# Kernel tuning notes

Hardware: AMD Instinct MI355X
Metric: run time of the kernel (lower is better)

The kernel has to match this reference:

```python
import jax, jax.numpy as jnp
import numpy as np

N = 50000      # nodes
E = 800000     # edges
F_IN = 128     # input node features
HID = 96       # hidden_channels (heads=1 -> in_dim=HID)
L = 4          # num_layers
OUT = 1
EPS_SM = 1e-16 # PyG softmax eps


def layer_norm(x, g, b):
    mu = jnp.mean(x, axis=-1, keepdims=True)
    var = jnp.var(x, axis=-1, keepdims=True)
    return (x - mu) * jax.lax.rsqrt(var + 1e-5) * g + b


def gatv2_layer(h, src, dst, ea, Wl, bl, Wr, br, We, att, bias):
    # GATv2Conv, heads=1, concat=True, add_self_loops=False, edge_dim=1
    xl = h @ Wl + bl                      # [N, C] source transform (x_j)
    xr = h @ Wr + br                      # [N, C] target transform (x_i)
    e = xl[src] + xr[dst] + ea @ We       # [E, C]
    e = jax.nn.leaky_relu(e, 0.2)
    alpha = e @ att                       # [E]
    # softmax over incoming edges of each destination node
    m = jax.ops.segment_max(alpha, dst, num_segments=N)
    a = jnp.exp(alpha - m[dst])
    s = jax.ops.segment_sum(a, dst, num_segments=N)
    a = a / (s[dst] + EPS_SM)
    out = jax.ops.segment_sum(xl[src] * a[:, None], dst, num_segments=N)
    return out + bias


def setup_inputs() -> dict:
    key = jax.random.key(0)
    ks = jax.random.split(key, 24)
    sc_in = 1.0 / np.sqrt(F_IN)
    sc_h = 1.0 / np.sqrt(HID)
    inp = {
        "x": jax.random.normal(ks[0], (N, F_IN), jnp.float32),
        "edge_index": jax.random.randint(ks[1], (2, E), 0, N, jnp.int64),
        "edge_weight": jax.random.uniform(ks[2], (E,), jnp.float32),
        "enc_W": jax.random.normal(ks[3], (F_IN, HID), jnp.float32) * sc_in,
        "enc_b": jnp.zeros((HID,), jnp.float32),
        "Wl": jax.random.normal(ks[4], (L, HID, HID), jnp.float32) * sc_h,
        "bl": jnp.zeros((L, HID), jnp.float32),
        "Wr": jax.random.normal(ks[5], (L, HID, HID), jnp.float32) * sc_h,
        "br": jnp.zeros((L, HID), jnp.float32),
        "We": jax.random.normal(ks[6], (L, 1, HID), jnp.float32),
        "att": jax.random.normal(ks[7], (L, HID), jnp.float32) * sc_h,
        "bias": jnp.zeros((L, HID), jnp.float32),
        "ln_g": jnp.ones((L, HID), jnp.float32),
        "ln_b": jnp.zeros((L, HID), jnp.float32),
        "lnf_g": jnp.ones((HID,), jnp.float32),
        "lnf_b": jnp.zeros((HID,), jnp.float32),
        "fc_W": jax.random.normal(ks[8], (HID, OUT), jnp.float32) * sc_h,
        "fc_b": jnp.zeros((OUT,), jnp.float32),
    }
    return inp


def reference(x, edge_index, edge_weight, enc_W, enc_b, Wl, bl, Wr, br, We, att,
              bias, ln_g, ln_b, lnf_g, lnf_b, fc_W, fc_b):
    src, dst = edge_index[0], edge_index[1]
    ea = edge_weight[:, None]             # [E, 1] edge_attr
    h = x @ enc_W + enc_b                 # node encoder
    for i in range(L):                    # DeepGCNLayer block='res+'
        hn = jax.nn.relu(layer_norm(h, ln_g[i], ln_b[i]))
        h = h + gatv2_layer(hn, src, dst, ea, Wl[i], bl[i], Wr[i], br[i],
                            We[i], att[i], bias[i])
    h = jax.nn.relu(layer_norm(h, lnf_g, lnf_b))
    return h @ fc_W + fc_b
```

## Files before the change

### kernel.cpp

```cpp
#include <hip/hip_runtime.h>
#include <math.h>

#define NN 50000
#define EE 800000
#define FIN 128
#define HID 96
#define NL 4
#define CHUNK 1024

typedef __attribute__((ext_vector_type(8))) short short8;
typedef __attribute__((ext_vector_type(4))) float floatx4;
typedef __attribute__((ext_vector_type(2))) _Float16 half2v;

#define WPREP_L (NL * 2 * 9216)
#define WPREP_TOT (WPREP_L + 12288)

#define PH1E 4096
#define NBUCK 98
#define BCAP 9216

struct u96 { unsigned x, y, z; };

__device__ __forceinline__ unsigned short f32_to_bf16_rne(float x) {
    unsigned u = __float_as_uint(x);
    unsigned r = (u + 0x7FFFu + ((u >> 16) & 1u)) >> 16;
    return (unsigned short)r;
}
__device__ __forceinline__ float bf16_to_f32(unsigned short h) {
    return __uint_as_float(((unsigned)h) << 16);
}

__global__ void k_hist(const int* __restrict__ dst, int* __restrict__ deg, int E) {
    int e = blockIdx.x * blockDim.x + threadIdx.x;
    if (e < E) atomicAdd(&deg[dst[e]], 1);
}

__global__ void k_scan1(const int* __restrict__ deg, int* __restrict__ partials, int n) {
    __shared__ int lds[256];
    int t = threadIdx.x;
    int base = blockIdx.x * CHUNK + t * 4;
    int s = 0;
    #pragma unroll
    for (int q = 0; q < 4; q++) { int idx = base + q; if (idx < n) s += deg[idx]; }
    lds[t] = s; __syncthreads();
    for (int o = 128; o > 0; o >>= 1) { if (t < o) lds[t] += lds[t + o]; __syncthreads(); }
    if (t == 0) partials[blockIdx.x] = lds[0];
}

__global__ void k_scan_mid(int* partials, int nb, int* rowptr, int n) {
    int lane = threadIdx.x;
    int orig = (lane < nb) ? partials[lane] : 0;
    int v = orig;
    #pragma unroll
    for (int off = 1; off < 64; off <<= 1) {
        int u = __shfl_up(v, off);
        if (lane >= off) v += u;
    }
    if (lane < nb) partials[lane] = v - orig;
    if (lane == 63) rowptr[n] = v;
}

__global__ void k_scan3(const int* __restrict__ deg, const int* __restrict__ partials,
                        int* __restrict__ rowptr, int* __restrict__ cursor, int n) {
    __shared__ int lds[256];
    int t = threadIdx.x;
    int base = blockIdx.x * CHUNK + t * 4;
    int v[4];
    #pragma unroll
    for (int q = 0; q < 4; q++) { int idx = base + q; v[q] = (idx < n) ? deg[idx] : 0; }
    int tsum = v[0] + v[1] + v[2] + v[3];
    lds[t] = tsum; __syncthreads();
    for (int o = 1; o < 256; o <<= 1) {
        int add = (t >= o) ? lds[t - o] : 0;
        __syncthreads();
        lds[t] += add;
        __syncthreads();
    }
    int excl = lds[t] - tsum;
    int run = partials[blockIdx.x] + excl;
    #pragma unroll
    for (int q = 0; q < 4; q++) {
        int idx = base + q;
        if (idx < n) { rowptr[idx] = run; cursor[idx] = run; run += v[q]; }
    }
}

__global__ __launch_bounds__(256) void k_binscatter(const int* __restrict__ src,
        const int* __restrict__ dst, const float* __restrict__ ew,
        int* __restrict__ gcur, uint2* __restrict__ ibuf, int E) {
    __shared__ uint2 st[PH1E];
    __shared__ int cnt[NBUCK], off[NBUCK], cur[NBUCK], gbase[NBUCK];
    int t = threadIdx.x;
    int e0 = blockIdx.x * PH1E;
    for (int i = t; i < NBUCK; i += 256) { cnt[i] = 0; cur[i] = 0; }
    __syncthreads();
    #pragma unroll
    for (int k = 0; k < PH1E / 256; k++) {
        int e = e0 + k * 256 + t;
        if (e < E) atomicAdd(&cnt[dst[e] >> 9], 1);
    }
    __syncthreads();
    if (t == 0) {
        int run = 0;
        for (int b = 0; b < NBUCK; b++) { off[b] = run; run += cnt[b]; }
    }
    __syncthreads();
    #pragma unroll
    for (int k = 0; k < PH1E / 256; k++) {
        int e = e0 + k * 256 + t;
        if (e < E) {
            int d = dst[e];
            int b = d >> 9;
            int p = off[b] + atomicAdd(&cur[b], 1);
            _Float16 hw = (_Float16)ew[e];
            unsigned short wb = *(unsigned short*)&hw;
            st[p] = make_uint2((unsigned)d, (unsigned)src[e] | ((unsigned)wb << 16));
        }
    }
    __syncthreads();
    if (t < NBUCK) gbase[t] = atomicAdd(&gcur[t], cur[t]);
    __syncthreads();
    int total = min(PH1E, E - e0);
    for (int i = t; i < total; i += 256) {
        uint2 v = st[i];
        int b = v.x >> 9;
        ibuf[(size_t)b * BCAP + gbase[b] + (i - off[b])] = v;
    }
}

__global__ __launch_bounds__(256) void k_binplace(const uint2* __restrict__ ibuf,
        const int* __restrict__ gcur, const int* __restrict__ rowptr,
        unsigned* __restrict__ epack, int n) {
    __shared__ int cur[512];
    int t = threadIdx.x;
    int b = blockIdx.x;
    int n0 = b << 9;
    for (int i = t; i < 512; i += 256) {
        int node = n0 + i;
        cur[i] = (node < n) ? rowptr[node] : 0;
    }
    __syncthreads();
    int nb = gcur[b];
    for (int i = t; i < nb; i += 256) {
        uint2 v = ibuf[(size_t)b * BCAP + i];
        int p = atomicAdd(&cur[(int)v.x - n0], 1);
        epack[p] = v.y;
    }
}

__global__ void k_wprep_all(const float* __restrict__ Wl, const float* __restrict__ Wr,
                            const float* __restrict__ encW,
                            unsigned short* __restrict__ wf_hi, unsigned short* __restrict__ wf_lo,
                            unsigned short* __restrict__ we_hi, unsigned short* __restrict__ we_lo) {
    int t = blockIdx.x * blockDim.x + threadIdx.x;
    if (t < WPREP_L) {
        int within = t % 9216, pair = t / 9216;
        int lr = pair & 1, layer = pair >> 1;
        int j = within & 7;
        int lane = (within >> 3) & 63;
        int cs = within >> 9;
        int s = cs % 3, ct = cs / 3;
        int col = ct * 16 + (lane & 15);
        int k = s * 32 + (lane >> 4) * 8 + j;
        const float* W = (lr ? Wr : Wl) + (size_t)layer * HID * HID;
        float v = W[k * HID + col];
        unsigned short hi = f32_to_bf16_rne(v);
        wf_hi[t] = hi;
        wf_lo[t] = f32_to_bf16_rne(v - bf16_to_f32(hi));
    } else if (t < WPREP_TOT) {
        int u = t - WPREP_L;
        int j = u & 7;
        int lane = (u >> 3) & 63;
        int cs = u >> 9;
        int s = cs & 3, ct = cs >> 2;
        int col = ct * 16 + (lane & 15);
        int k = s * 32 + (lane >> 4) * 8 + j;
        float v = encW[k * HID + col];
        unsigned short hi = f32_to_bf16_rne(v);
        we_hi[u] = hi;
        we_lo[u] = f32_to_bf16_rne(v - bf16_to_f32(hi));
    }
}

__global__ __launch_bounds__(256) void k_enc_mfma(const float* __restrict__ x,
        const unsigned short* __restrict__ we_hi, const unsigned short* __restrict__ we_lo,
        const float* __restrict__ b,
        const float* __restrict__ lng, const float* __restrict__ lnb,
        float* __restrict__ h,
        unsigned short* __restrict__ hn_hi, unsigned short* __restrict__ hn_lo, int n) {
    int t = threadIdx.x;
    int wave = t >> 6, lane = t & 63;
    int quad = lane >> 4, lid = lane & 15;
    int r0 = blockIdx.x * 64 + wave * 16;
    int arow = r0 + lid; if (arow >= n) arow = n - 1;
    short8 aH[4], aL[4];
    #pragma unroll
    for (int s = 0; s < 4; s++) {
        float4 p0 = *(const float4*)(x + (size_t)arow * FIN + s * 32 + quad * 8);
        float4 p1 = *(const float4*)(x + (size_t)arow * FIN + s * 32 + quad * 8 + 4);
        float f[8] = {p0.x, p0.y, p0.z, p0.w, p1.x, p1.y, p1.z, p1.w};
        #pragma unroll
        for (int j = 0; j < 8; j++) {
            unsigned short hi = f32_to_bf16_rne(f[j]);
            aH[s][j] = (short)hi;
            aL[s][j] = (short)f32_to_bf16_rne(f[j] - bf16_to_f32(hi));
        }
    }
    floatx4 o[6];
    #pragma unroll
    for (int ct = 0; ct < 6; ct++) {
        floatx4 acc = {0.f, 0.f, 0.f, 0.f};
        #pragma unroll
        for (int s = 0; s < 4; s++) {
            short8 bH = *(const short8*)(we_hi + ((ct * 4 + s) * 64 + lane) * 8);
            short8 bL = *(const short8*)(we_lo + ((ct * 4 + s) * 64 + lane) * 8);
            acc = __builtin_amdgcn_mfma_f32_16x16x32_bf16(aH[s], bH, acc, 0, 0, 0);
            acc = __builtin_amdgcn_mfma_f32_16x16x32_bf16(aH[s], bL, acc, 0, 0, 0);
            acc = __builtin_amdgcn_mfma_f32_16x16x32_bf16(aL[s], bH, acc, 0, 0, 0);
        }
        float bv = b[ct * 16 + lid];
        #pragma unroll
        for (int rg = 0; rg < 4; rg++) o[ct][rg] = acc[rg] + bv;
    }
    #pragma unroll
    for (int rg = 0; rg < 4; rg++) {
        float s1 = 0.f, s2 = 0.f;
        #pragma unroll
        for (int ct = 0; ct < 6; ct++) { s1 += o[ct][rg]; s2 += o[ct][rg] * o[ct][rg]; }
        #pragma unroll
        for (int off = 1; off < 16; off <<= 1) {
            s1 += __shfl_xor(s1, off);
            s2 += __shfl_xor(s2, off);
        }
        float mu = s1 * (1.f / 96.f);
        float var = s2 * (1.f / 96.f) - mu * mu;
        float rs = rsqrtf(var + 1e-5f);
        int orow = r0 + quad * 4 + rg;
        if (orow < n) {
            #pragma unroll
            for (int ct = 0; ct < 6; ct++) {
                int col = ct * 16 + lid;
                float v = o[ct][rg];
                h[(size_t)orow * HID + col] = v;
                float y = fmaxf((v - mu) * rs * lng[col] + lnb[col], 0.f);
                unsigned short hi = f32_to_bf16_rne(y);
                hn_hi[(size_t)orow * HID + col] = hi;
                hn_lo[(size_t)orow * HID + col] = f32_to_bf16_rne(y - bf16_to_f32(hi));
            }
        }
    }
}

__global__ __launch_bounds__(256) void k_gemm2_mfma(
        const unsigned short* __restrict__ hn_hi, const unsigned short* __restrict__ hn_lo,
        const unsigned short* __restrict__ wf_hi, const unsigned short* __restrict__ wf_lo,
        const float* __restrict__ bl, const float* __restrict__ br,
        unsigned short* __restrict__ xl_h, unsigned short* __restrict__ xr_h, int n) {
    __shared__ unsigned short lh[9216];
    __shared__ unsigned short ll[9216];
    int t = threadIdx.x;
    int wave = t >> 6, lane = t & 63;
    int quad = lane >> 4, lid = lane & 15;
    int r0 = blockIdx.x * 64 + wave * 16;
    int arow = r0 + lid; if (arow >= n) arow = n - 1;
    short8 aH[3], aL[3];
    #pragma unroll
    for (int s = 0; s < 3; s++) {
        aH[s] = *(const short8*)(hn_hi + (size_t)arow * HID + s * 32 + quad * 8);
        aL[s] = *(const short8*)(hn_lo + (size_t)arow * HID + s * 32 + quad * 8);
    }
    for (int lr = 0; lr < 2; lr++) {
        const unsigned short* sh = wf_hi + lr * 9216;
        const unsigned short* sl = wf_lo + lr * 9216;
        __syncthreads();
        for (int u = t; u < 1152; u += 256) {
            *(short8*)(lh + u * 8) = *(const short8*)(sh + u * 8);
            *(short8*)(ll + u * 8) = *(const short8*)(sl + u * 8);
        }
        __syncthreads();
        const float* bias = lr ? br : bl;
        unsigned short* out = lr ? xr_h : xl_h;
        #pragma unroll
        for (int ct = 0; ct < 6; ct++) {
            floatx4 acc = {0.f, 0.f, 0.f, 0.f};
            #pragma unroll
            for (int s = 0; s < 3; s++) {
                short8 bH = *(const short8*)(lh + ((ct * 3 + s) * 64 + lane) * 8);
                short8 bL = *(const short8*)(ll + ((ct * 3 + s) * 64 + lane) * 8);
                acc = __builtin_amdgcn_mfma_f32_16x16x32_bf16(aH[s], bH, acc, 0, 0, 0);
                acc = __builtin_amdgcn_mfma_f32_16x16x32_bf16(aH[s], bL, acc, 0, 0, 0);
                acc = __builtin_amdgcn_mfma_f32_16x16x32_bf16(aL[s], bH, acc, 0, 0, 0);
            }
            int col = ct * 16 + lid;
            float bv = bias[col];
            #pragma unroll
            for (int rg = 0; rg < 4; rg++) {
                int orow = r0 + quad * 4 + rg;
                if (orow < n) {
                    _Float16 hv = (_Float16)(acc[rg] + bv);
                    out[(size_t)orow * HID + col] = *(unsigned short*)&hv;
                }
            }
        }
    }
}

__global__ __launch_bounds__(256) void k_gat_fused(
        const unsigned short* __restrict__ xl_h, const unsigned short* __restrict__ xr_h,
        const unsigned* __restrict__ ep, const int* __restrict__ rowptr,
        const float* __restrict__ We, const float* __restrict__ att, const float* __restrict__ bias,
        float* __restrict__ h,
        unsigned short* __restrict__ hn_hi, unsigned short* __restrict__ hn_lo,
        float* __restrict__ out_final,
        const float* __restrict__ g, const float* __restrict__ bt,
        const float* __restrict__ fcW, const float* __restrict__ fcb,
        int mode, int n) {
    int lane = threadIdx.x & 63;
    int node = blockIdx.x * 4 + (threadIdx.x >> 6);
    if (node >= n) return;
    int grp = lane >> 4, sub = lane & 15;
    int d0 = sub * 6;
    unsigned gOffB = (unsigned)(sub * 12);

    const float LOG2E = 1.4426950408889634f;
    union U6 { u96 u; half2v h2[3]; _Float16 hf[6]; };
    half2v we_h[3], at_h[3], xr_hv[3];
    {
        U6 xrw;
        xrw.u = *(const u96*)((const char*)xr_h + ((unsigned)node * 192u + gOffB));
        float2 a0 = *(const float2*)(We + d0);
        float2 a1 = *(const float2*)(We + d0 + 2);
        float2 a2 = *(const float2*)(We + d0 + 4);
        float2 c0 = *(const float2*)(att + d0);
        float2 c1 = *(const float2*)(att + d0 + 2);
        float2 c2 = *(const float2*)(att + d0 + 4);
        we_h[0] = half2v{(_Float16)a0.x, (_Float16)a0.y};
        we_h[1] = half2v{(_Float16)a1.x, (_Float16)a1.y};
        we_h[2] = half2v{(_Float16)a2.x, (_Float16)a2.y};
        at_h[0] = half2v{(_Float16)(c0.x*LOG2E), (_Float16)(c0.y*LOG2E)};
        at_h[1] = half2v{(_Float16)(c1.x*LOG2E), (_Float16)(c1.y*LOG2E)};
        at_h[2] = half2v{(_Float16)(c2.x*LOG2E), (_Float16)(c2.y*LOG2E)};
        #pragma unroll
        for (int j = 0; j < 3; j++) xr_hv[j] = xrw.h2[j];
    }
    const half2v c02 = half2v{(_Float16)0.2f, (_Float16)0.2f};

    int beg = rowptr[node], end = rowptr[node + 1];
    float ssum = 0.f;
    float acc[6];
    #pragma unroll
    for (int j = 0; j < 6; j++) acc[j] = 0.f;

    auto lq = [&](int p, u96& vraw, _Float16& wh, bool& val) {
        int pe = p + grp;
        val = pe < end;
        int pc = val ? pe : end - 1;
        unsigned e = ep[pc];
        unsigned short wb = (unsigned short)(e >> 16);
        wh = *(_Float16*)&wb;
        vraw = *(const u96*)((const char*)xl_h + ((e & 0xFFFFu) * 192u + gOffB));
    };
    auto proc = [&](const u96& vraw, _Float16 wh, bool val) {
        U6 cv; cv.u = vraw;
        half2v w2 = half2v{wh, wh};
        float q = 0.f;
        #pragma unroll
        for (int j = 0; j < 3; j++) {
            half2v t = cv.h2[j] + xr_hv[j];
            t = w2 * we_h[j] + t;
            half2v t2 = t * c02;
            t = __builtin_elementwise_max(t, t2);
#if __has_builtin(__builtin_amdgcn_fdot2)
            q = __builtin_amdgcn_fdot2(t, at_h[j], q, false);
#else
            q = fmaf((float)t[0], (float)at_h[j][0], q);
            q = fmaf((float)t[1], (float)at_h[j][1], q);
#endif
        }
        q += __shfl_xor(q, 1); q += __shfl_xor(q, 2);
        q += __shfl_xor(q, 4); q += __shfl_xor(q, 8);
        float e = val ? exp2f(q) : 0.f;
        ssum += e;
        #pragma unroll
        for (int j = 0; j < 6; j++) acc[j] = fmaf((float)cv.hf[j], e, acc[j]);
    };

    if (beg < end) {
        u96 vA, vB; _Float16 wA, wB; bool okA, okB;
        lq(beg,     vA, wA, okA);
        lq(beg + 4, vB, wB, okB);
        for (int p = beg; p < end; p += 8) {
            proc(vA, wA, okA);
            lq(p + 8, vA, wA, okA);
            proc(vB, wB, okB);
            lq(p + 12, vB, wB, okB);
        }
    }

    ssum += __shfl_xor(ssum, 16); ssum += __shfl_xor(ssum, 32);
    #pragma unroll
    for (int j = 0; j < 6; j++) {
        acc[j] += __shfl_xor(acc[j], 16);
        acc[j] += __shfl_xor(acc[j], 32);
    }
    float inv = 1.f / (ssum + 1e-16f);

    float nh[6];
    float s1 = 0.f, s2 = 0.f;
    {
        float2 h0 = *(const float2*)(h + (size_t)node * HID + d0);
        float2 h1 = *(const float2*)(h + (size_t)node * HID + d0 + 2);
        float2 h2 = *(const float2*)(h + (size_t)node * HID + d0 + 4);
        float2 b0 = *(const float2*)(bias + d0);
        float2 b1 = *(const float2*)(bias + d0 + 2);
        float2 b2 = *(const float2*)(bias + d0 + 4);
        float hv[6] = {h0.x, h0.y, h1.x, h1.y, h2.x, h2.y};
        float bv[6] = {b0.x, b0.y, b1.x, b1.y, b2.x, b2.y};
        #pragma unroll
        for (int j = 0; j < 6; j++) {
            nh[j] = hv[j] + acc[j] * inv + bv[j];
            s1 += nh[j];
            s2 += nh[j] * nh[j];
        }
    }
    #pragma unroll
    for (int off = 1; off < 16; off <<= 1) {
        s1 += __shfl_xor(s1, off);
        s2 += __shfl_xor(s2, off);
    }
    float mu = s1 * (1.f / 96.f);
    float var = s2 * (1.f / 96.f) - mu * mu;
    float rs = rsqrtf(var + 1e-5f);

    if (mode == 0) {
        if (grp == 0) {
            float2 g0 = *(const float2*)(g + d0);
            float2 g1 = *(const float2*)(g + d0 + 2);
            float2 g2 = *(const float2*)(g + d0 + 4);
            float2 t0 = *(const float2*)(bt + d0);
            float2 t1 = *(const float2*)(bt + d0 + 2);
            float2 t2 = *(const float2*)(bt + d0 + 4);
            float gv[6] = {g0.x, g0.y, g1.x, g1.y, g2.x, g2.y};
            float tv[6] = {t0.x, t0.y, t1.x, t1.y, t2.x, t2.y};
            *(float2*)(h + (size_t)node * HID + d0)     = make_float2(nh[0], nh[1]);
            *(float2*)(h + (size_t)node * HID + d0 + 2) = make_float2(nh[2], nh[3]);
            *(float2*)(h + (size_t)node * HID + d0 + 4) = make_float2(nh[4], nh[5]);
            unsigned hi[3], lo[3];
            #pragma unroll
            for (int j = 0; j < 3; j++) {
                float ox = fmaxf((nh[2*j]   - mu) * rs * gv[2*j]   + tv[2*j],   0.f);
                float oy = fmaxf((nh[2*j+1] - mu) * rs * gv[2*j+1] + tv[2*j+1], 0.f);
                unsigned short hx = f32_to_bf16_rne(ox), hy = f32_to_bf16_rne(oy);
                unsigned short lx = f32_to_bf16_rne(ox - bf16_to_f32(hx));
                unsigned short ly = f32_to_bf16_rne(oy - bf16_to_f32(hy));
                hi[j] = (unsigned)hx | ((unsigned)hy << 16);
                lo[j] = (unsigned)lx | ((unsigned)ly << 16);
            }
            u96 wh = {hi[0], hi[1], hi[2]};
            u96 wl = {lo[0], lo[1], lo[2]};
            *(u96*)((char*)hn_hi + 2 * ((size_t)node * HID + d0)) = wh;
            *(u96*)((char*)hn_lo + 2 * ((size_t)node * HID + d0)) = wl;
        }
    } else {
        float pacc = 0.f;
        {
            float2 g0 = *(const float2*)(g + d0);
            float2 g1 = *(const float2*)(g + d0 + 2);
            float2 g2 = *(const float2*)(g + d0 + 4);
            float2 t0 = *(const float2*)(bt + d0);
            float2 t1 = *(const float2*)(bt + d0 + 2);
            float2 t2 = *(const float2*)(bt + d0 + 4);
            float2 w0 = *(const float2*)(fcW + d0);
            float2 w1 = *(const float2*)(fcW + d0 + 2);
            float2 w2 = *(const float2*)(fcW + d0 + 4);
            float gv[6] = {g0.x, g0.y, g1.x, g1.y, g2.x, g2.y};
            float tv[6] = {t0.x, t0.y, t1.x, t1.y, t2.x, t2.y};
            float wv[6] = {w0.x, w0.y, w1.x, w1.y, w2.x, w2.y};
            #pragma unroll
            for (int j = 0; j < 6; j++) {
                float y = fmaxf((nh[j] - mu) * rs * gv[j] + tv[j], 0.f);
                pacc = fmaf(y, wv[j], pacc);
            }
        }
        #pragma unroll
        for (int off = 1; off < 16; off <<= 1) pacc += __shfl_xor(pacc, off);
        if (lane == 0) out_final[node] = pacc + fcb[0];
    }
}

extern "C" void kernel_launch(void* const* d_in, const int* in_sizes, int n_in,
                              void* d_out, int out_size, void* d_ws, size_t ws_size,
                              hipStream_t stream) {
    const float* x    = (const float*)d_in[0];
    const int*   ei   = (const int*)  d_in[1];
    const float* ew   = (const float*)d_in[2];
    const float* encW = (const float*)d_in[3];
    const float* encB = (const float*)d_in[4];
    const float* Wl   = (const float*)d_in[5];
    const float* bl   = (const float*)d_in[6];
    const float* Wr   = (const float*)d_in[7];
    const float* br   = (const float*)d_in[8];
    const float* We   = (const float*)d_in[9];
    const float* att  = (const float*)d_in[10];
    const float* bias = (const float*)d_in[11];
    const float* lng  = (const float*)d_in[12];
    const float* lnb  = (const float*)d_in[13];
    const float* lnfg = (const float*)d_in[14];
    const float* lnfb = (const float*)d_in[15];
    const float* fcW  = (const float*)d_in[16];
    const float* fcb  = (const float*)d_in[17];
    float* out = (float*)d_out;

    const int* src = ei;
    const int* dst = ei + EE;

    char* ws = (char*)d_ws;
    size_t off = 0;
    auto alloc = [&](size_t bytes) -> void* {
        void* p = ws + off;
        off += (bytes + 255) & ~(size_t)255;
        return p;
    };
    float* h      = (float*)alloc((size_t)NN * HID * 4);
    unsigned short* xl_h  = (unsigned short*)alloc((size_t)NN * HID * 2 + 256);
    unsigned short* xr_h  = (unsigned short*)alloc((size_t)NN * HID * 2 + 256);
    unsigned short* hn_hi = (unsigned short*)alloc((size_t)NN * HID * 2);
    unsigned short* hn_lo = (unsigned short*)alloc((size_t)NN * HID * 2);
    unsigned short* wf_hi = (unsigned short*)alloc((size_t)WPREP_L * 2);
    unsigned short* wf_lo = (unsigned short*)alloc((size_t)WPREP_L * 2);
    unsigned short* we_hi = (unsigned short*)alloc(12288 * 2);
    unsigned short* we_lo = (unsigned short*)alloc(12288 * 2);
    int*   deg    = (int*)  alloc((size_t)NN * 4);
    int*   rowptr = (int*)  alloc((size_t)(NN + 1) * 4);
    int*   cursor = (int*)  alloc((size_t)NN * 4);
    unsigned* epack = (unsigned*)alloc((size_t)EE * 4);
    uint2* ibuf   = (uint2*)alloc((size_t)NBUCK * BCAP * 8);
    int*   gcur   = (int*)  alloc(NBUCK * 4);
    int*   parts  = (int*)  alloc(256 * 4);

    const int NB = (NN + CHUNK - 1) / CHUNK;
    const int EB = (EE + 255) / 256;
    const int PB = (EE + PH1E - 1) / PH1E;
    const int MB = (NN + 63) / 64;
    const int WB = (NN + 3) / 4;

    hipMemsetAsync(deg, 0, (size_t)NN * 4, stream);
    hipMemsetAsync(gcur, 0, NBUCK * 4, stream);
    k_hist<<<EB, 256, 0, stream>>>(dst, deg, EE);
    k_binscatter<<<PB, 256, 0, stream>>>(src, dst, ew, gcur, ibuf, EE);
    k_scan1<<<NB, 256, 0, stream>>>(deg, parts, NN);
    k_scan_mid<<<1, 64, 0, stream>>>(parts, NB, rowptr, NN);
    k_scan3<<<NB, 256, 0, stream>>>(deg, parts, rowptr, cursor, NN);
    k_binplace<<<NBUCK, 256, 0, stream>>>(ibuf, gcur, rowptr, epack, NN);

    k_wprep_all<<<(WPREP_TOT + 255) / 256, 256, 0, stream>>>(Wl, Wr, encW, wf_hi, wf_lo, we_hi, we_lo);

    k_enc_mfma<<<MB, 256, 0, stream>>>(x, we_hi, we_lo, encB, lng, lnb, h, hn_hi, hn_lo, NN);

    for (int l = 0; l < NL; l++) {
        k_gemm2_mfma<<<MB, 256, 0, stream>>>(hn_hi, hn_lo,
            wf_hi + (size_t)l * 2 * 9216, wf_lo + (size_t)l * 2 * 9216,
            bl + l * HID, br + l * HID, xl_h, xr_h, NN);
        if (l < NL - 1) {
            k_gat_fused<<<WB, 256, 0, stream>>>(xl_h, xr_h, epack, rowptr,
                We + l * HID, att + l * HID, bias + l * HID,
                h, hn_hi, hn_lo, (float*)nullptr,
                lng + (l + 1) * HID, lnb + (l + 1) * HID,
                (const float*)nullptr, (const float*)nullptr, 0, NN);
        } else {
            k_gat_fused<<<WB, 256, 0, stream>>>(xl_h, xr_h, epack, rowptr,
                We + l * HID, att + l * HID, bias + l * HID,
                h, (unsigned short*)nullptr, (unsigned short*)nullptr, out,
                lnfg, lnfb, fcW, fcb, 1, NN);
        }
    }
}
```

Measured before the change: 451.3 us.

## Replace split-bf16 triple MFMA with single fp16 MFMA and fold degree histogram

Switches the node encoder and per-layer dual GEMMs from a hi/lo bf16 split (three MFMAs per step, two activation buffers, two weight copies) to one fp16 MFMA with a single fp16 activation and weight buffer. This halves hn read/write traffic in the GAT epilogue and GEMM, halves LDS weight staging, and cuts MFMA count by a factor of three. It also moves the in-degree histogram into the bin-scatter kernel, dropping one launch and one extra pass over dst. The cost is lower matmul precision (fp16 with 10-bit mantissa instead of near-fp32 split) and possible fp16 range limits.

```diff
diff --git a/kernel.cpp b/kernel.cpp
--- a/kernel.cpp
+++ b/kernel.cpp
@@ -21,18 +21,9 @@
 
 struct u96 { unsigned x, y, z; };
 
-__device__ __forceinline__ unsigned short f32_to_bf16_rne(float x) {
-    unsigned u = __float_as_uint(x);
-    unsigned r = (u + 0x7FFFu + ((u >> 16) & 1u)) >> 16;
-    return (unsigned short)r;
-}
-__device__ __forceinline__ float bf16_to_f32(unsigned short h) {
-    return __uint_as_float(((unsigned)h) << 16);
-}
-
-__global__ void k_hist(const int* __restrict__ dst, int* __restrict__ deg, int E) {
-    int e = blockIdx.x * blockDim.x + threadIdx.x;
-    if (e < E) atomicAdd(&deg[dst[e]], 1);
+__device__ __forceinline__ unsigned short f16bits(float x) {
+    _Float16 h = (_Float16)x;
+    return *(unsigned short*)&h;
 }
 
 __global__ void k_scan1(const int* __restrict__ deg, int* __restrict__ partials, int n) {
@@ -87,7 +78,7 @@
 
 __global__ __launch_bounds__(256) void k_binscatter(const int* __restrict__ src,
         const int* __restrict__ dst, const float* __restrict__ ew,
-        int* __restrict__ gcur, uint2* __restrict__ ibuf, int E) {
+        int* __restrict__ deg, int* __restrict__ gcur, uint2* __restrict__ ibuf, int E) {
     __shared__ uint2 st[PH1E];
     __shared__ int cnt[NBUCK], off[NBUCK], cur[NBUCK], gbase[NBUCK];
     int t = threadIdx.x;
@@ -97,7 +88,11 @@
     #pragma unroll
     for (int k = 0; k < PH1E / 256; k++) {
         int e = e0 + k * 256 + t;
-        if (e < E) atomicAdd(&cnt[dst[e] >> 9], 1);
+        if (e < E) {
+            int d = dst[e];
+            atomicAdd(&cnt[d >> 9], 1);
+            atomicAdd(&deg[d], 1);
+        }
     }
     __syncthreads();
     if (t == 0) {
@@ -112,8 +107,7 @@
             int d = dst[e];
             int b = d >> 9;
             int p = off[b] + atomicAdd(&cur[b], 1);
-            _Float16 hw = (_Float16)ew[e];
-            unsigned short wb = *(unsigned short*)&hw;
+            unsigned short wb = f16bits(ew[e]);
             st[p] = make_uint2((unsigned)d, (unsigned)src[e] | ((unsigned)wb << 16));
         }
     }
@@ -150,8 +144,7 @@
 
 __global__ void k_wprep_all(const float* __restrict__ Wl, const float* __restrict__ Wr,
                             const float* __restrict__ encW,
-                            unsigned short* __restrict__ wf_hi, unsigned short* __restrict__ wf_lo,
-                            unsigned short* __restrict__ we_hi, unsigned short* __restrict__ we_lo) {
+                            unsigned short* __restrict__ wf, unsigned short* __restrict__ we) {
     int t = blockIdx.x * blockDim.x + threadIdx.x;
     if (t < WPREP_L) {
         int within = t % 9216, pair = t / 9216;
@@ -163,10 +156,7 @@
         int col = ct * 16 + (lane & 15);
         int k = s * 32 + (lane >> 4) * 8 + j;
         const float* W = (lr ? Wr : Wl) + (size_t)layer * HID * HID;
-        float v = W[k * HID + col];
-        unsigned short hi = f32_to_bf16_rne(v);
-        wf_hi[t] = hi;
-        wf_lo[t] = f32_to_bf16_rne(v - bf16_to_f32(hi));
+        wf[t] = f16bits(W[k * HID + col]);
     } else if (t < WPREP_TOT) {
         int u = t - WPREP_L;
         int j = u & 7;
@@ -175,36 +165,29 @@
         int s = cs & 3, ct = cs >> 2;
         int col = ct * 16 + (lane & 15);
         int k = s * 32 + (lane >> 4) * 8 + j;
-        float v = encW[k * HID + col];
-        unsigned short hi = f32_to_bf16_rne(v);
-        we_hi[u] = hi;
-        we_lo[u] = f32_to_bf16_rne(v - bf16_to_f32(hi));
+        we[u] = f16bits(encW[k * HID + col]);
     }
 }
 
 __global__ __launch_bounds__(256) void k_enc_mfma(const float* __restrict__ x,
-        const unsigned short* __restrict__ we_hi, const unsigned short* __restrict__ we_lo,
+        const unsigned short* __restrict__ we,
         const float* __restrict__ b,
         const float* __restrict__ lng, const float* __restrict__ lnb,
         float* __restrict__ h,
-        unsigned short* __restrict__ hn_hi, unsigned short* __restrict__ hn_lo, int n) {
+        unsigned short* __restrict__ hn, int n) {
     int t = threadIdx.x;
     int wave = t >> 6, lane = t & 63;
     int quad = lane >> 4, lid = lane & 15;
     int r0 = blockIdx.x * 64 + wave * 16;
     int arow = r0 + lid; if (arow >= n) arow = n - 1;
-    short8 aH[4], aL[4];
+    short8 aF[4];
     #pragma unroll
     for (int s = 0; s < 4; s++) {
         float4 p0 = *(const float4*)(x + (size_t)arow * FIN + s * 32 + quad * 8);
         float4 p1 = *(const float4*)(x + (size_t)arow * FIN + s * 32 + quad * 8 + 4);
         float f[8] = {p0.x, p0.y, p0.z, p0.w, p1.x, p1.y, p1.z, p1.w};
         #pragma unroll
-        for (int j = 0; j < 8; j++) {
-            unsigned short hi = f32_to_bf16_rne(f[j]);
-            aH[s][j] = (short)hi;
-            aL[s][j] = (short)f32_to_bf16_rne(f[j] - bf16_to_f32(hi));
-        }
+        for (int j = 0; j < 8; j++) aF[s][j] = (short)f16bits(f[j]);
     }
     floatx4 o[6];
     #pragma unroll
@@ -212,11 +195,8 @@
         floatx4 acc = {0.f, 0.f, 0.f, 0.f};
         #pragma unroll
         for (int s = 0; s < 4; s++) {
-            short8 bH = *(const short8*)(we_hi + ((ct * 4 + s) * 64 + lane) * 8);
-            short8 bL = *(const short8*)(we_lo + ((ct * 4 + s) * 64 + lane) * 8);
-            acc = __builtin_amdgcn_mfma_f32_16x16x32_bf16(aH[s], bH, acc, 0, 0, 0);
-            acc = __builtin_amdgcn_mfma_f32_16x16x32_bf16(aH[s], bL, acc, 0, 0, 0);
-            acc = __builtin_amdgcn_mfma_f32_16x16x32_bf16(aL[s], bH, acc, 0, 0, 0);
+            short8 bF = *(const short8*)(we + ((ct * 4 + s) * 64 + lane) * 8);
+            acc = __builtin_amdgcn_mfma_f32_16x16x32_f16(aF[s], bF, acc, 0, 0, 0);
         }
         float bv = b[ct * 16 + lid];
         #pragma unroll
@@ -243,40 +223,32 @@
                 float v = o[ct][rg];
                 h[(size_t)orow * HID + col] = v;
                 float y = fmaxf((v - mu) * rs * lng[col] + lnb[col], 0.f);
-                unsigned short hi = f32_to_bf16_rne(y);
-                hn_hi[(size_t)orow * HID + col] = hi;
-                hn_lo[(size_t)orow * HID + col] = f32_to_bf16_rne(y - bf16_to_f32(hi));
+                hn[(size_t)orow * HID + col] = f16bits(y);
             }
         }
     }
 }
 
 __global__ __launch_bounds__(256) void k_gemm2_mfma(
-        const unsigned short* __restrict__ hn_hi, const unsigned short* __restrict__ hn_lo,
-        const unsigned short* __restrict__ wf_hi, const unsigned short* __restrict__ wf_lo,
+        const unsigned short* __restrict__ hn,
+        const unsigned short* __restrict__ wf,
         const float* __restrict__ bl, const float* __restrict__ br,
         unsigned short* __restrict__ xl_h, unsigned short* __restrict__ xr_h, int n) {
-    __shared__ unsigned short lh[9216];
-    __shared__ unsigned short ll[9216];
+    __shared__ unsigned short lw[9216];
     int t = threadIdx.x;
     int wave = t >> 6, lane = t & 63;
     int quad = lane >> 4, lid = lane & 15;
     int r0 = blockIdx.x * 64 + wave * 16;
     int arow = r0 + lid; if (arow >= n) arow = n - 1;
-    short8 aH[3], aL[3];
-    #pragma unroll
-    for (int s = 0; s < 3; s++) {
-        aH[s] = *(const short8*)(hn_hi + (size_t)arow * HID + s * 32 + quad * 8);
-        aL[s] = *(const short8*)(hn_lo + (size_t)arow * HID + s * 32 + quad * 8);
-    }
+    short8 aF[3];
+    #pragma unroll
+    for (int s = 0; s < 3; s++)
+        aF[s] = *(const short8*)(hn + (size_t)arow * HID + s * 32 + quad * 8);
     for (int lr = 0; lr < 2; lr++) {
-        const unsigned short* sh = wf_hi + lr * 9216;
-        const unsigned short* sl = wf_lo + lr * 9216;
+        const unsigned short* sw = wf + lr * 9216;
         __syncthreads();
-        for (int u = t; u < 1152; u += 256) {
-            *(short8*)(lh + u * 8) = *(const short8*)(sh + u * 8);
-            *(short8*)(ll + u * 8) = *(const short8*)(sl + u * 8);
-        }
+        for (int u = t; u < 1152; u += 256)
+            *(short8*)(lw + u * 8) = *(const short8*)(sw + u * 8);
         __syncthreads();
         const float* bias = lr ? br : bl;
         unsigned short* out = lr ? xr_h : xl_h;
@@ -285,21 +257,15 @@
             floatx4 acc = {0.f, 0.f, 0.f, 0.f};
             #pragma unroll
             for (int s = 0; s < 3; s++) {
-                short8 bH = *(const short8*)(lh + ((ct * 3 + s) * 64 + lane) * 8);
-                short8 bL = *(const short8*)(ll + ((ct * 3 + s) * 64 + lane) * 8);
-                acc = __builtin_amdgcn_mfma_f32_16x16x32_bf16(aH[s], bH, acc, 0, 0, 0);
-                acc = __builtin_amdgcn_mfma_f32_16x16x32_bf16(aH[s], bL, acc, 0, 0, 0);
-                acc = __builtin_amdgcn_mfma_f32_16x16x32_bf16(aL[s], bH, acc, 0, 0, 0);
+                short8 bF = *(const short8*)(lw + ((ct * 3 + s) * 64 + lane) * 8);
+                acc = __builtin_amdgcn_mfma_f32_16x16x32_f16(aF[s], bF, acc, 0, 0, 0);
             }
             int col = ct * 16 + lid;
             float bv = bias[col];
             #pragma unroll
             for (int rg = 0; rg < 4; rg++) {
                 int orow = r0 + quad * 4 + rg;
-                if (orow < n) {
-                    _Float16 hv = (_Float16)(acc[rg] + bv);
-                    out[(size_t)orow * HID + col] = *(unsigned short*)&hv;
-                }
+                if (orow < n) out[(size_t)orow * HID + col] = f16bits(acc[rg] + bv);
             }
         }
     }
@@ -310,7 +276,7 @@
         const unsigned* __restrict__ ep, const int* __restrict__ rowptr,
         const float* __restrict__ We, const float* __restrict__ att, const float* __restrict__ bias,
         float* __restrict__ h,
-        unsigned short* __restrict__ hn_hi, unsigned short* __restrict__ hn_lo,
+        unsigned short* __restrict__ hn,
         float* __restrict__ out_final,
         const float* __restrict__ g, const float* __restrict__ bt,
         const float* __restrict__ fcW, const float* __restrict__ fcb,
@@ -445,21 +411,15 @@
             *(float2*)(h + (size_t)node * HID + d0)     = make_float2(nh[0], nh[1]);
             *(float2*)(h + (size_t)node * HID + d0 + 2) = make_float2(nh[2], nh[3]);
             *(float2*)(h + (size_t)node * HID + d0 + 4) = make_float2(nh[4], nh[5]);
-            unsigned hi[3], lo[3];
+            unsigned w[3];
             #pragma unroll
             for (int j = 0; j < 3; j++) {
                 float ox = fmaxf((nh[2*j]   - mu) * rs * gv[2*j]   + tv[2*j],   0.f);
                 float oy = fmaxf((nh[2*j+1] - mu) * rs * gv[2*j+1] + tv[2*j+1], 0.f);
-                unsigned short hx = f32_to_bf16_rne(ox), hy = f32_to_bf16_rne(oy);
-                unsigned short lx = f32_to_bf16_rne(ox - bf16_to_f32(hx));
-                unsigned short ly = f32_to_bf16_rne(oy - bf16_to_f32(hy));
-                hi[j] = (unsigned)hx | ((unsigned)hy << 16);
-                lo[j] = (unsigned)lx | ((unsigned)ly << 16);
+                w[j] = (unsigned)f16bits(ox) | ((unsigned)f16bits(oy) << 16);
             }
-            u96 wh = {hi[0], hi[1], hi[2]};
-            u96 wl = {lo[0], lo[1], lo[2]};
-            *(u96*)((char*)hn_hi + 2 * ((size_t)node * HID + d0)) = wh;
-            *(u96*)((char*)hn_lo + 2 * ((size_t)node * HID + d0)) = wl;
+            u96 wv6 = {w[0], w[1], w[2]};
+            *(u96*)((char*)hn + 2 * ((size_t)node * HID + d0)) = wv6;
         }
     } else {
         float pacc = 0.f;
@@ -524,12 +484,9 @@
     float* h      = (float*)alloc((size_t)NN * HID * 4);
     unsigned short* xl_h  = (unsigned short*)alloc((size_t)NN * HID * 2 + 256);
     unsigned short* xr_h  = (unsigned short*)alloc((size_t)NN * HID * 2 + 256);
-    unsigned short* hn_hi = (unsigned short*)alloc((size_t)NN * HID * 2);
-    unsigned short* hn_lo = (unsigned short*)alloc((size_t)NN * HID * 2);
-    unsigned short* wf_hi = (unsigned short*)alloc((size_t)WPREP_L * 2);
-    unsigned short* wf_lo = (unsigned short*)alloc((size_t)WPREP_L * 2);
-    unsigned short* we_hi = (unsigned short*)alloc(12288 * 2);
-    unsigned short* we_lo = (unsigned short*)alloc(12288 * 2);
+    unsigned short* hn    = (unsigned short*)alloc((size_t)NN * HID * 2 + 256);
+    unsigned short* wf    = (unsigned short*)alloc((size_t)WPREP_L * 2);
+    unsigned short* we    = (unsigned short*)alloc(12288 * 2);
     int*   deg    = (int*)  alloc((size_t)NN * 4);
     int*   rowptr = (int*)  alloc((size_t)(NN + 1) * 4);
     int*   cursor = (int*)  alloc((size_t)NN * 4);
@@ -539,38 +496,36 @@
     int*   parts  = (int*)  alloc(256 * 4);
 
     const int NB = (NN + CHUNK - 1) / CHUNK;
-    const int EB = (EE + 255) / 256;
     const int PB = (EE + PH1E - 1) / PH1E;
     const int MB = (NN + 63) / 64;
     const int WB = (NN + 3) / 4;
 
     hipMemsetAsync(deg, 0, (size_t)NN * 4, stream);
     hipMemsetAsync(gcur, 0, NBUCK * 4, stream);
-    k_hist<<<EB, 256, 0, stream>>>(dst, deg, EE);
-    k_binscatter<<<PB, 256, 0, stream>>>(src, dst, ew, gcur, ibuf, EE);
+    k_binscatter<<<PB, 256, 0, stream>>>(src, dst, ew, deg, gcur, ibuf, EE);
     k_scan1<<<NB, 256, 0, stream>>>(deg, parts, NN);
     k_scan_mid<<<1, 64, 0, stream>>>(parts, NB, rowptr, NN);
     k_scan3<<<NB, 256, 0, stream>>>(deg, parts, rowptr, cursor, NN);
     k_binplace<<<NBUCK, 256, 0, stream>>>(ibuf, gcur, rowptr, epack, NN);
 
-    k_wprep_all<<<(WPREP_TOT + 255) / 256, 256, 0, stream>>>(Wl, Wr, encW, wf_hi, wf_lo, we_hi, we_lo);
-
-    k_enc_mfma<<<MB, 256, 0, stream>>>(x, we_hi, we_lo, encB, lng, lnb, h, hn_hi, hn_lo, NN);
+    k_wprep_all<<<(WPREP_TOT + 255) / 256, 256, 0, stream>>>(Wl, Wr, encW, wf, we);
+
+    k_enc_mfma<<<MB, 256, 0, stream>>>(x, we, encB, lng, lnb, h, hn, NN);
 
     for (int l = 0; l < NL; l++) {
-        k_gemm2_mfma<<<MB, 256, 0, stream>>>(hn_hi, hn_lo,
-            wf_hi + (size_t)l * 2 * 9216, wf_lo + (size_t)l * 2 * 9216,
+        k_gemm2_mfma<<<MB, 256, 0, stream>>>(hn,
+            wf + (size_t)l * 2 * 9216,
             bl + l * HID, br + l * HID, xl_h, xr_h, NN);
         if (l < NL - 1) {
             k_gat_fused<<<WB, 256, 0, stream>>>(xl_h, xr_h, epack, rowptr,
                 We + l * HID, att + l * HID, bias + l * HID,
-                h, hn_hi, hn_lo, (float*)nullptr,
+                h, hn, (float*)nullptr,
                 lng + (l + 1) * HID, lnb + (l + 1) * HID,
                 (const float*)nullptr, (const float*)nullptr, 0, NN);
         } else {
             k_gat_fused<<<WB, 256, 0, stream>>>(xl_h, xr_h, epack, rowptr,
                 We + l * HID, att + l * HID, bias + l * HID,
-                h, (unsigned short*)nullptr, (unsigned short*)nullptr, out,
+                h, (unsigned short*)nullptr, out,
                 lnfg, lnfb, fcW, fcb, 1, NN);
         }
     }
```

Result: faster. 435.4 us (-3.5%).
